# Kernel optimization log

Hardware: AMD Instinct MI355X
Metric: run time of the kernel (lower is better)

The kernel has to match this reference:

```python
import jax, jax.numpy as jnp
import numpy as np

B, T, E, H, V, K = 32, 256, 256, 256, 32000, 48
PAD = 0


def setup_inputs() -> dict:
    key = jax.random.key(0)
    ks = jax.random.split(key, 24)
    lengths = jnp.sort(jax.random.randint(ks[0], (B,), 1, T + 1))[::-1]
    lengths = lengths.at[0].set(T)  # pack_padded needs max length present
    sent = jax.random.randint(ks[1], (B, T), 1, V)
    pos = jnp.arange(T)[None, :]
    sentence = jnp.where(pos < lengths[:, None], sent, PAD)
    tags = jax.random.randint(ks[2], (B, T), 0, K)
    s = 0.1
    p = {"sentence": sentence, "lengths": lengths, "tags": tags}
    p["embed"] = jax.random.normal(ks[3], (V, E)) * s
    dims = [E, 2 * H]
    i = 4
    for l in range(2):
        for d in ("f", "b"):
            p[f"Wih_{l}{d}"] = jax.random.normal(ks[i], (4 * H, dims[l])) * s; i += 1
            p[f"Whh_{l}{d}"] = jax.random.normal(ks[i], (4 * H, H)) * s; i += 1
            p[f"b_{l}{d}"] = jax.random.normal(ks[i], (4 * H,)) * s; i += 1
    p["Wout"] = jax.random.normal(ks[i], (K, 2 * H)) * s; i += 1
    p["bout"] = jax.random.normal(ks[i], (K,)) * s; i += 1
    p["start_t"] = jax.random.normal(ks[i], (K,)) * s; i += 1
    p["end_t"] = jax.random.normal(ks[i], (K,)) * s; i += 1
    p["trans"] = jax.random.normal(ks[i], (K, K)) * s
    return p


def _lstm_dir(x, m, Wih, Whh, b, reverse):
    # x: [T,B,D] time-major, m: [T,B] bool. Masked update emulates pack_padded_sequence.
    if reverse:
        x, m = x[::-1], m[::-1]
    Bn, Hn = x.shape[1], Whh.shape[1]

    def step(carry, inp):
        h, c = carry
        xt, mt = inp
        g = xt @ Wih.T + h @ Whh.T + b
        i_, f_, g_, o_ = jnp.split(g, 4, axis=-1)
        c2 = jax.nn.sigmoid(f_) * c + jax.nn.sigmoid(i_) * jnp.tanh(g_)
        h2 = jax.nn.sigmoid(o_) * jnp.tanh(c2)
        mm = mt[:, None]
        h2 = jnp.where(mm, h2, h)
        c2 = jnp.where(mm, c2, c)
        return (h2, c2), jnp.where(mm, h2, 0.0)

    init = (jnp.zeros((Bn, Hn), x.dtype), jnp.zeros((Bn, Hn), x.dtype))
    _, hs = jax.lax.scan(step, init, (x, m))
    return hs[::-1] if reverse else hs


def _forward(sentence, tags, embed, layer_params, Wout, bout, start_t, end_t, trans):
    mask = sentence != PAD                      # [B,T]
    x = embed[sentence]                          # [B,T,E]
    xt = jnp.transpose(x, (1, 0, 2))             # [T,B,E]
    mt = mask.T                                  # [T,B]
    for (Wf, Uf, bf, Wb, Ub, bb) in layer_params:
        hf = _lstm_dir(xt, mt, Wf, Uf, bf, False)
        hb = _lstm_dir(xt, mt, Wb, Ub, bb, True)
        xt = jnp.concatenate([hf, hb], axis=-1)  # [T,B,2H]
    emit = xt @ Wout.T + bout                    # [T,B,K]; dropout is identity in eval

    # ---- CRF log-likelihood (torchcrf) ----
    mf = mt.astype(emit.dtype)
    tt = tags.T                                  # [T,B]
    bar = jnp.arange(sentence.shape[0])
    num = start_t[tt[0]] + emit[0, bar, tt[0]]

    def num_step(s, inp):
        em, tg, pg, m = inp
        return s + (trans[pg, tg] + em[bar, tg]) * m, None

    num, _ = jax.lax.scan(num_step, num, (emit[1:], tt[1:], tt[:-1], mf[1:]))
    last_idx = mf.sum(0).astype(jnp.int32) - 1
    last_tags = tt[last_idx, bar]
    num = num + end_t[last_tags]

    score = start_t[None, :] + emit[0]           # [B,K]

    def den_step(s, inp):
        em, m = inp
        nxt = jax.nn.logsumexp(s[:, :, None] + trans[None] + em[:, None, :], axis=1)
        return jnp.where(m[:, None] > 0, nxt, s), None

    score, _ = jax.lax.scan(den_step, score, (emit[1:], mf[1:]))
    den = jax.nn.logsumexp(score + end_t[None, :], axis=1)
    loss = (num - den).mean()                    # torchcrf reduction='mean' log-likelihood
    return jnp.transpose(emit, (1, 0, 2)), loss, mask


def reference(sentence, lengths, tags, embed,
              Wih_0f, Whh_0f, b_0f, Wih_0b, Whh_0b, b_0b,
              Wih_1f, Whh_1f, b_1f, Wih_1b, Whh_1b, b_1b,
              Wout, bout, start_t, end_t, trans):
    layers = [(Wih_0f, Whh_0f, b_0f, Wih_0b, Whh_0b, b_0b),
              (Wih_1f, Whh_1f, b_1f, Wih_1b, Whh_1b, b_1b)]
    return _forward(sentence, tags, embed, layers, Wout, bout, start_t, end_t, trans)
```

## Files before the change

kernel.cpp:

```cpp
#include <hip/hip_runtime.h>

#define Bz 32
#define Tz 256
#define Ez 256
#define Hz 256
#define Kz 48
#define G4 1024
#define H2 512

typedef __attribute__((ext_vector_type(8))) short short8;
typedef __attribute__((ext_vector_type(4))) float f32x4;
typedef unsigned short ushort_t;
typedef unsigned int uint_t;
typedef unsigned long long ull_t;

__device__ __forceinline__ float bf2f(ushort_t u) {
    unsigned int x = ((unsigned int)u) << 16;
    union { unsigned int i; float f; } c; c.i = x; return c.f;
}
__device__ __forceinline__ ushort_t f2bf(float f) {
    union { float f; unsigned int i; } c; c.f = f;
    unsigned int x = c.i;
    unsigned int lsb = (x >> 16) & 1u;
    x += 0x7fffu + lsb;
    return (ushort_t)(x >> 16);
}
__device__ __forceinline__ float sigm(float x) { return 1.f / (1.f + __expf(-x)); }
__device__ __forceinline__ float tanh_f(float x) { return 1.f - 2.f / (__expf(2.f * x) + 1.f); }

#define MFMA16(a, b, c) __builtin_amdgcn_mfma_f32_16x16x32_bf16((a), (b), (c), 0, 0, 0)

struct CvtArgs {
    const float* s[9];
    ushort_t* d[9];
    int n[9];
};
__global__ __launch_bounds__(256) void cvt_all(CvtArgs a)
{
    int y = blockIdx.y;
    const float* src = a.s[y];
    ushort_t* dst = a.d[y];
    int n = a.n[y];
    int i = (blockIdx.x * 256 + threadIdx.x) * 4;
    if (i < n) {
        float4 v = *(const float4*)(src + i);
        ushort_t o[4] = { f2bf(v.x), f2bf(v.y), f2bf(v.z), f2bf(v.w) };
        *(uint2*)(dst + i) = *(uint2*)o;
    }
}

__global__ __launch_bounds__(64) void embed_kernel(
    const int* __restrict__ sent, const float* __restrict__ embed,
    ushort_t* __restrict__ emb, float* __restrict__ mask_out)
{
    int blk = blockIdx.x;
    int b = blk >> 8, t = blk & 255;
    int s = sent[blk];
    int tid = threadIdx.x;
    float4 v = *(const float4*)(embed + (size_t)s * Ez + tid * 4);
    ushort_t o[4] = { f2bf(v.x), f2bf(v.y), f2bf(v.z), f2bf(v.w) };
    *(uint2*)(emb + ((size_t)t * Bz + b) * Ez + tid * 4) = *(uint2*)o;
    if (tid == 0) mask_out[blk] = (s != 0) ? 1.0f : 0.0f;
}

__global__ __launch_bounds__(256) void gemm_xproj(
    const ushort_t* __restrict__ A,
    const ushort_t* __restrict__ Wf, const ushort_t* __restrict__ Wb,
    const float* __restrict__ biasf, const float* __restrict__ biasb,
    ushort_t* __restrict__ Cf, ushort_t* __restrict__ Cb,
    int M, int Kd)
{
    const ushort_t* W = blockIdx.z ? Wb : Wf;
    const float* bias = blockIdx.z ? biasb : biasf;
    ushort_t* C = blockIdx.z ? Cb : Cf;
    __shared__ __attribute__((aligned(16))) ushort_t sA[128 * 32];
    __shared__ __attribute__((aligned(16))) ushort_t sB[128 * 32];

    int m0 = blockIdx.x * 128, n0 = blockIdx.y * 128;
    int tid = threadIdx.x, l = tid & 63, w = tid >> 6;
    int lr = l & 15, lq = l >> 4;
    int mw = (w & 1) * 64, nw = (w >> 1) * 64;

    int srow_lane = l >> 2;
    int scol_lane = (l & 3) * 8;

    f32x4 acc[4][4] = {};
    for (int ko = 0; ko < Kd; ko += 32) {
        #pragma unroll
        for (int j = 0; j < 4; j++) {
            int seg = w * 4 + j;
            const ushort_t* src;
            ushort_t* dst;
            if (seg < 8) {
                src = A + (size_t)(m0 + seg * 16 + srow_lane) * Kd + ko + scol_lane;
                dst = sA + seg * 512;
            } else {
                src = W + (size_t)(n0 + (seg - 8) * 16 + srow_lane) * Kd + ko + scol_lane;
                dst = sB + (seg - 8) * 512;
            }
            __builtin_amdgcn_global_load_lds(src, dst, 16, 0, 0);
        }
        asm volatile("s_waitcnt vmcnt(0)" ::: "memory");
        __syncthreads();

        short8 af[4], bf_[4];
        #pragma unroll
        for (int mt = 0; mt < 4; mt++)
            af[mt] = *(const short8*)(&sA[(mw + mt * 16 + lr) * 32 + lq * 8]);
        #pragma unroll
        for (int nt = 0; nt < 4; nt++)
            bf_[nt] = *(const short8*)(&sB[(nw + nt * 16 + lr) * 32 + lq * 8]);
        #pragma unroll
        for (int mt = 0; mt < 4; mt++)
            #pragma unroll
            for (int nt = 0; nt < 4; nt++)
                acc[mt][nt] = MFMA16(af[mt], bf_[nt], acc[mt][nt]);
        __syncthreads();
    }

    #pragma unroll
    for (int mt = 0; mt < 4; mt++)
        #pragma unroll
        for (int nt = 0; nt < 4; nt++)
            #pragma unroll
            for (int r = 0; r < 4; r++) {
                int row = m0 + mw + mt * 16 + lq * 4 + r;
                int col = n0 + nw + nt * 16 + lr;
                float v = acc[mt][nt][r] + bias[col];
                C[(size_t)row * G4 + col] = f2bf(v);
            }
}

#define LDK 264

__global__ __launch_bounds__(256, 1) void lstm_layer(
    const ushort_t* __restrict__ Whh_f, const ushort_t* __restrict__ Whh_b,
    const ushort_t* __restrict__ Xp_f, const ushort_t* __restrict__ Xp_b,
    const int* __restrict__ lengths,
    ushort_t* __restrict__ hcat,
    ull_t* __restrict__ hbuf)
{
    __shared__ __attribute__((aligned(16))) ushort_t sH[Bz][LDK];
    __shared__ float sG[4][16][34];

    int bid = blockIdx.x;
    int dir = bid >> 4;
    int sub = bid & 15;
    int h0 = sub * 16;
    const ushort_t* Whh = dir ? Whh_b : Whh_f;
    const ushort_t* Xp  = dir ? Xp_b  : Xp_f;
    int tid = threadIdx.x, l = tid & 63, w = tid >> 6;
    int lr = l & 15, lq = l >> 4;
    int mw = (w & 1) * 16;
    int P  = w >> 1;
    int U0w = h0 + P * 8;

    short8 bw0[8], bw1[8];
    int gA = (lr & 3) * Hz + U0w + (lr >> 2);
    int gB = gA + 4;
    {
        const ushort_t* W0 = Whh + (size_t)gA * Hz;
        const ushort_t* W1 = Whh + (size_t)gB * Hz;
        #pragma unroll
        for (int k = 0; k < 8; k++) {
            bw0[k] = *(const short8*)(W0 + k * 32 + lq * 8);
            bw1[k] = *(const short8*)(W1 + k * 32 + lq * 8);
        }
    }

    int upd = (l < 32);
    int bloc = l & 15;
    int q = (l >> 4) & 1;
    int batch = mw + bloc;
    int lenb = lengths[batch];
    float c4[4] = {0.f, 0.f, 0.f, 0.f};
    ull_t prevw = 0;
    int pubw = batch * 64 + sub * 4 + P * 2 + q;
    int hcoff = dir * Hz + U0w + q * 4;

    for (int s = 0; s < Tz; s++) {
        int t_act = dir ? (Tz - 1 - s) : s;
        const ushort_t* Xrow = Xp + (size_t)t_act * Bz * G4;

        float xv0[4], xv1[4];
        #pragma unroll
        for (int r = 0; r < 4; r++) {
            int brow = mw + lq * 4 + r;
            xv0[r] = bf2f(Xrow[(size_t)brow * G4 + gA]);
            xv1[r] = bf2f(Xrow[(size_t)brow * G4 + gB]);
        }

        const ull_t* hcur = hbuf + ((s & 1) * 2 + dir) * (Bz * Hz / 4);
        uint_t tagc = (uint_t)(((s >> 1) ^ s) & 1);
        ull_t vals[8];
        uint_t pend = 0xffu;
        while (pend) {
            #pragma unroll
            for (int k = 0; k < 8; k++)
                if (pend & (1u << k))
                    vals[k] = __hip_atomic_load(&hcur[k * 256 + tid],
                                                __ATOMIC_RELAXED, __HIP_MEMORY_SCOPE_AGENT);
            #pragma unroll
            for (int k = 0; k < 8; k++)
                if ((pend & (1u << k)) && (((uint_t)(vals[k] >> 14) & 1u) == tagc))
                    pend &= ~(1u << k);
        }
        #pragma unroll
        for (int k = 0; k < 8; k++) {
            int idx = k * 256 + tid;
            *(ull_t*)(&sH[idx >> 6][(idx & 63) * 4]) = vals[k] & ~(1ull << 14);
        }
        __syncthreads();

        f32x4 acc0 = {}, acc1 = {};
        #pragma unroll
        for (int k = 0; k < 8; k++) {
            short8 a = *(const short8*)(&sH[mw + lr][k * 32 + lq * 8]);
            acc0 = MFMA16(a, bw0[k], acc0);
            acc1 = MFMA16(a, bw1[k], acc1);
        }
        #pragma unroll
        for (int r = 0; r < 4; r++) {
            sG[w][lq * 4 + r][lr]      = acc0[r] + xv0[r];
            sG[w][lq * 4 + r][16 + lr] = acc1[r] + xv1[r];
        }
        asm volatile("s_waitcnt lgkmcnt(0)" ::: "memory");

        uint_t tagp = (uint_t)((((s + 1) >> 1) ^ (s + 1)) & 1);
        if (upd) {
            int msk = (t_act < lenb);
            ushort_t hx[4], hc[4];
            const ushort_t* ho = (const ushort_t*)&prevw;
            #pragma unroll
            for (int j = 0; j < 4; j++) {
                int cb = q * 16 + j * 4;
                float gi = sG[w][bloc][cb], gf = sG[w][bloc][cb + 1];
                float gg = sG[w][bloc][cb + 2], go = sG[w][bloc][cb + 3];
                float c2 = sigm(gf) * c4[j] + sigm(gi) * tanh_f(gg);
                float h2 = sigm(go) * tanh_f(c2);
                if (msk) c4[j] = c2;
                ushort_t hn = f2bf(h2);
                hx[j] = msk ? hn : ho[j];
                hc[j] = msk ? hn : (ushort_t)0;
            }
            ull_t wd; __builtin_memcpy(&wd, hx, 8);
            prevw = wd;
            wd |= ((ull_t)tagp) << 14;
            ull_t* hnxt = hbuf + (((s + 1) & 1) * 2 + dir) * (Bz * Hz / 4);
            __hip_atomic_store(&hnxt[pubw], wd,
                               __ATOMIC_RELAXED, __HIP_MEMORY_SCOPE_AGENT);
            ull_t wc; __builtin_memcpy(&wc, hc, 8);
            *(ull_t*)(hcat + ((size_t)t_act * Bz + batch) * H2 + hcoff) = wc;
        }
    }
}

__global__ __launch_bounds__(256) void gemm_emit(
    const ushort_t* __restrict__ A, const ushort_t* __restrict__ Wout,
    const float* __restrict__ bout, float* __restrict__ emit_out)
{
    int tid = threadIdx.x, l = tid & 63, w = tid >> 6;
    int m0 = blockIdx.x * 64 + w * 16;
    int lr = l & 15, lq = l >> 4;
    f32x4 acc[3] = {};
    for (int ko = 0; ko < H2; ko += 32) {
        short8 a = *(const short8*)(A + (size_t)(m0 + lr) * H2 + ko + lq * 8);
        #pragma unroll
        for (int nt = 0; nt < 3; nt++) {
            short8 bfr = *(const short8*)(Wout + (size_t)(nt * 16 + lr) * H2 + ko + lq * 8);
            acc[nt] = MFMA16(a, bfr, acc[nt]);
        }
    }
    #pragma unroll
    for (int nt = 0; nt < 3; nt++)
        #pragma unroll
        for (int r = 0; r < 4; r++) {
            int row = m0 + lq * 4 + r;
            int col = nt * 16 + lr;
            float v = acc[nt][r] + bout[col];
            int t = row >> 5, b = row & 31;
            emit_out[((size_t)b * Tz + t) * Kz + col] = v;
        }
}

__global__ __launch_bounds__(256) void crf_num(
    const float* __restrict__ emit, const int* __restrict__ sent,
    const int* __restrict__ tags, const int* __restrict__ lengths,
    const float* __restrict__ trans, const float* __restrict__ start_t,
    const float* __restrict__ end_t, float* __restrict__ num)
{
    __shared__ float red[4];
    int b = blockIdx.x, t = threadIdx.x;
    int tg = tags[b * Tz + t];
    float term;
    if (t == 0) {
        term = start_t[tg] + emit[(size_t)b * Tz * Kz + tg];
        int len = lengths[b];
        term += end_t[tags[b * Tz + len - 1]];
    } else if (sent[b * Tz + t] != 0) {
        int tp = tags[b * Tz + t - 1];
        term = trans[tp * Kz + tg] + emit[((size_t)b * Tz + t) * Kz + tg];
    } else term = 0.f;
    #pragma unroll
    for (int off = 1; off < 64; off <<= 1) term += __shfl_xor(term, off);
    int w = t >> 6;
    if ((t & 63) == 0) red[w] = term;
    __syncthreads();
    if (t == 0) num[b] = red[0] + red[1] + red[2] + red[3];
}

__global__ __launch_bounds__(64) void crf_den(
    const float* __restrict__ emit, const int* __restrict__ lengths,
    const float* __restrict__ trans, const float* __restrict__ start_t,
    const float* __restrict__ end_t, float* __restrict__ den)
{
    __shared__ float sT[Kz * Kz];
    __shared__ float sS[Kz];
    int b = blockIdx.x, l = threadIdx.x;
    for (int i = l; i < Kz * Kz; i += 64) sT[i] = trans[i];
    int len = lengths[b];
    bool act = l < Kz;
    float s = act ? (start_t[l] + emit[(size_t)b * Tz * Kz + l]) : -1e30f;
    for (int t = 1; t < len; t++) {
        float em = act ? emit[((size_t)b * Tz + t) * Kz + l] : 0.f;
        if (act) sS[l] = s;
        float M = s;
        #pragma unroll
        for (int off = 1; off < 64; off <<= 1) M = fmaxf(M, __shfl_xor(M, off));
        float a0 = 0.f, a1 = 0.f, a2 = 0.f, a3 = 0.f;
        #pragma unroll 4
        for (int i = 0; i < Kz; i += 4) {
            a0 += __expf(sS[i]     + sT[i * Kz + l]       - M);
            a1 += __expf(sS[i + 1] + sT[(i + 1) * Kz + l] - M);
            a2 += __expf(sS[i + 2] + sT[(i + 2) * Kz + l] - M);
            a3 += __expf(sS[i + 3] + sT[(i + 3) * Kz + l] - M);
        }
        float sum = (a0 + a1) + (a2 + a3);
        if (act) s = em + M + __logf(sum);
    }
    float v = act ? (s + end_t[l]) : -1e30f;
    float M = v;
    #pragma unroll
    for (int off = 1; off < 64; off <<= 1) M = fmaxf(M, __shfl_xor(M, off));
    float accv = act ? __expf(v - M) : 0.f;
    #pragma unroll
    for (int off = 1; off < 64; off <<= 1) accv += __shfl_xor(accv, off);
    if (l == 0) den[b] = M + __logf(accv);
}

__global__ __launch_bounds__(64) void crf_loss(
    const float* __restrict__ num, const float* __restrict__ den, float* __restrict__ out)
{
    int l = threadIdx.x;
    float v = (l < Bz) ? (num[l] - den[l]) : 0.f;
    #pragma unroll
    for (int off = 1; off < 64; off <<= 1) v += __shfl_xor(v, off);
    if (l == 0) out[0] = v / (float)Bz;
}

extern "C" void kernel_launch(void* const* d_in, const int* in_sizes, int n_in,
                              void* d_out, int out_size, void* d_ws, size_t ws_size,
                              hipStream_t stream) {
    const int* sent      = (const int*)d_in[0];
    const int* lengths   = (const int*)d_in[1];
    const int* tags      = (const int*)d_in[2];
    const float* embed   = (const float*)d_in[3];
    const float* Wih0f = (const float*)d_in[4];
    const float* Whh0f = (const float*)d_in[5];
    const float* b0f   = (const float*)d_in[6];
    const float* Wih0b = (const float*)d_in[7];
    const float* Whh0b = (const float*)d_in[8];
    const float* b0b   = (const float*)d_in[9];
    const float* Wih1f = (const float*)d_in[10];
    const float* Whh1f = (const float*)d_in[11];
    const float* b1f   = (const float*)d_in[12];
    const float* Wih1b = (const float*)d_in[13];
    const float* Whh1b = (const float*)d_in[14];
    const float* b1b   = (const float*)d_in[15];
    const float* Wout  = (const float*)d_in[16];
    const float* bout  = (const float*)d_in[17];
    const float* start_t = (const float*)d_in[18];
    const float* end_t   = (const float*)d_in[19];
    const float* trans   = (const float*)d_in[20];

    char* ws = (char*)d_ws;
    ushort_t* Xp_f  = (ushort_t*)(ws);
    ushort_t* Xp_b  = (ushort_t*)(ws + 16777216);
    ushort_t* hcat  = (ushort_t*)(ws + 33554432);
    ushort_t* emb   = (ushort_t*)(ws + 41943040);
    ushort_t* Whh0f_c = (ushort_t*)(ws + 46137344);
    ushort_t* Whh0b_c = (ushort_t*)(ws + 46661632);
    ushort_t* Wih0f_c = (ushort_t*)(ws + 47185920);
    ushort_t* Wih0b_c = (ushort_t*)(ws + 47710208);
    ushort_t* Wih1f_c = (ushort_t*)(ws + 48234496);
    ushort_t* Wih1b_c = (ushort_t*)(ws + 49283072);
    ushort_t* Whh1f_c = (ushort_t*)(ws + 50331648);
    ushort_t* Whh1b_c = (ushort_t*)(ws + 50855936);
    ushort_t* Wout_c  = (ushort_t*)(ws + 51380224);
    ull_t*    hbufL0 = (ull_t*)(ws + 51429376);
    ull_t*    hbufL1 = (ull_t*)(ws + 51560448);
    float*    num   = (float*)   (ws + 51691520);
    float*    den   = (float*)   (ws + 51691776);

    float* out      = (float*)d_out;
    float* loss_out = out + (size_t)Bz * Tz * Kz;
    float* mask_out = loss_out + 1;

    hipMemsetAsync(hbufL0, 0, 262144, stream);

    CvtArgs ca;
    ca.s[0] = Whh0f; ca.d[0] = Whh0f_c; ca.n[0] = 262144;
    ca.s[1] = Whh0b; ca.d[1] = Whh0b_c; ca.n[1] = 262144;
    ca.s[2] = Wih0f; ca.d[2] = Wih0f_c; ca.n[2] = 262144;
    ca.s[3] = Wih0b; ca.d[3] = Wih0b_c; ca.n[3] = 262144;
    ca.s[4] = Wih1f; ca.d[4] = Wih1f_c; ca.n[4] = 524288;
    ca.s[5] = Wih1b; ca.d[5] = Wih1b_c; ca.n[5] = 524288;
    ca.s[6] = Whh1f; ca.d[6] = Whh1f_c; ca.n[6] = 262144;
    ca.s[7] = Whh1b; ca.d[7] = Whh1b_c; ca.n[7] = 262144;
    ca.s[8] = Wout;  ca.d[8] = Wout_c;  ca.n[8] = 24576;
    cvt_all<<<dim3(512, 9), 256, 0, stream>>>(ca);

    embed_kernel<<<Bz * Tz, 64, 0, stream>>>(sent, embed, emb, mask_out);

    gemm_xproj<<<dim3(Tz * Bz / 128, G4 / 128, 2), 256, 0, stream>>>(
        emb, Wih0f_c, Wih0b_c, b0f, b0b, Xp_f, Xp_b, Tz * Bz, Ez);

    lstm_layer<<<32, 256, 0, stream>>>(Whh0f_c, Whh0b_c, Xp_f, Xp_b, lengths, hcat, hbufL0);

    gemm_xproj<<<dim3(Tz * Bz / 128, G4 / 128, 2), 256, 0, stream>>>(
        hcat, Wih1f_c, Wih1b_c, b1f, b1b, Xp_f, Xp_b, Tz * Bz, H2);

    lstm_layer<<<32, 256, 0, stream>>>(Whh1f_c, Whh1b_c, Xp_f, Xp_b, lengths, hcat, hbufL1);

    gemm_emit<<<Tz * Bz / 64, 256, 0, stream>>>(hcat, Wout_c, bout, out);

    crf_num<<<Bz, 256, 0, stream>>>(out, sent, tags, lengths, trans, start_t, end_t, num);
    crf_den<<<Bz, 64, 0, stream>>>(out, lengths, trans, start_t, end_t, den);
    crf_loss<<<1, 64, 0, stream>>>(num, den, loss_out);
}
```

Baseline: 1.877 ms.

## Replace per-word tag polling with per-wave step flags in LSTM recurrence

Cross-block synchronisation of the hidden state switches from spinning on tag bits embedded in every published h word to spinning on two per-wave step-counter flags, then loading h once. Each wave waits for its stores to drain (vmcnt(0)) and lane 0 publishes the step number as a flag. This cuts the polling traffic per thread from eight words to two flags, at the cost of an extra store-drain and flag write per step. Ordering between the h stores and the flag uses relaxed atomics plus a waitcnt rather than a release/acquire pair, so visibility depends on hardware ordering.

```diff
diff --git a/kernel.cpp b/kernel.cpp
--- a/kernel.cpp
+++ b/kernel.cpp
@@ -138,7 +138,8 @@
     const ushort_t* __restrict__ Xp_f, const ushort_t* __restrict__ Xp_b,
     const int* __restrict__ lengths,
     ushort_t* __restrict__ hcat,
-    ull_t* __restrict__ hbuf)
+    ull_t* __restrict__ hbuf,
+    ull_t* __restrict__ flags)
 {
     __shared__ __attribute__((aligned(16))) ushort_t sH[Bz][LDK];
     __shared__ float sG[4][16][34];
@@ -177,6 +178,10 @@
     ull_t prevw = 0;
     int pubw = batch * 64 + sub * 4 + P * 2 + q;
     int hcoff = dir * Hz + U0w + q * 4;
+    int wr = tid & 63;
+    int slotA = (wr & ~3) | (wr & 2);
+    int slotB = slotA + 1;
+    int myflag = sub * 4 + w;
 
     for (int s = 0; s < Tz; s++) {
         int t_act = dir ? (Tz - 1 - s) : s;
@@ -190,25 +195,30 @@
             xv1[r] = bf2f(Xrow[(size_t)brow * G4 + gB]);
         }
 
+        const ull_t* fb = flags + ((s & 1) * 2 + dir) * 64;
+        ull_t se = (ull_t)s;
+        uint_t need = 3u;
+        while (need) {
+            if (need & 1u) {
+                ull_t fA = __hip_atomic_load(&fb[slotA],
+                                             __ATOMIC_RELAXED, __HIP_MEMORY_SCOPE_AGENT);
+                if (fA == se) need &= ~1u;
+            }
+            if (need & 2u) {
+                ull_t fB = __hip_atomic_load(&fb[slotB],
+                                             __ATOMIC_RELAXED, __HIP_MEMORY_SCOPE_AGENT);
+                if (fB == se) need &= ~2u;
+            }
+        }
+        asm volatile("" ::: "memory");
+
         const ull_t* hcur = hbuf + ((s & 1) * 2 + dir) * (Bz * Hz / 4);
-        uint_t tagc = (uint_t)(((s >> 1) ^ s) & 1);
-        ull_t vals[8];
-        uint_t pend = 0xffu;
-        while (pend) {
-            #pragma unroll
-            for (int k = 0; k < 8; k++)
-                if (pend & (1u << k))
-                    vals[k] = __hip_atomic_load(&hcur[k * 256 + tid],
-                                                __ATOMIC_RELAXED, __HIP_MEMORY_SCOPE_AGENT);
-            #pragma unroll
-            for (int k = 0; k < 8; k++)
-                if ((pend & (1u << k)) && (((uint_t)(vals[k] >> 14) & 1u) == tagc))
-                    pend &= ~(1u << k);
-        }
         #pragma unroll
         for (int k = 0; k < 8; k++) {
+            ull_t v = __hip_atomic_load(&hcur[k * 256 + tid],
+                                        __ATOMIC_RELAXED, __HIP_MEMORY_SCOPE_AGENT);
             int idx = k * 256 + tid;
-            *(ull_t*)(&sH[idx >> 6][(idx & 63) * 4]) = vals[k] & ~(1ull << 14);
+            *(ull_t*)(&sH[idx >> 6][(idx & 63) * 4]) = v;
         }
         __syncthreads();
 
@@ -226,7 +236,6 @@
         }
         asm volatile("s_waitcnt lgkmcnt(0)" ::: "memory");
 
-        uint_t tagp = (uint_t)((((s + 1) >> 1) ^ (s + 1)) & 1);
         if (upd) {
             int msk = (t_act < lenb);
             ushort_t hx[4], hc[4];
@@ -245,12 +254,17 @@
             }
             ull_t wd; __builtin_memcpy(&wd, hx, 8);
             prevw = wd;
-            wd |= ((ull_t)tagp) << 14;
             ull_t* hnxt = hbuf + (((s + 1) & 1) * 2 + dir) * (Bz * Hz / 4);
             __hip_atomic_store(&hnxt[pubw], wd,
                                __ATOMIC_RELAXED, __HIP_MEMORY_SCOPE_AGENT);
             ull_t wc; __builtin_memcpy(&wc, hc, 8);
             *(ull_t*)(hcat + ((size_t)t_act * Bz + batch) * H2 + hcoff) = wc;
+        }
+        asm volatile("s_waitcnt vmcnt(0)" ::: "memory");
+        if (l == 0) {
+            ull_t* fn = flags + (((s + 1) & 1) * 2 + dir) * 64;
+            __hip_atomic_store(&fn[myflag], (ull_t)(s + 1),
+                               __ATOMIC_RELAXED, __HIP_MEMORY_SCOPE_AGENT);
         }
     }
 }
@@ -399,14 +413,16 @@
     ushort_t* Wout_c  = (ushort_t*)(ws + 51380224);
     ull_t*    hbufL0 = (ull_t*)(ws + 51429376);
     ull_t*    hbufL1 = (ull_t*)(ws + 51560448);
-    float*    num   = (float*)   (ws + 51691520);
-    float*    den   = (float*)   (ws + 51691776);
+    ull_t*    flagsL0 = (ull_t*)(ws + 51691520);
+    ull_t*    flagsL1 = (ull_t*)(ws + 51693568);
+    float*    num   = (float*)   (ws + 51695616);
+    float*    den   = (float*)   (ws + 51695872);
 
     float* out      = (float*)d_out;
     float* loss_out = out + (size_t)Bz * Tz * Kz;
     float* mask_out = loss_out + 1;
 
-    hipMemsetAsync(hbufL0, 0, 262144, stream);
+    hipMemsetAsync(hbufL0, 0, 266240, stream);
 
     CvtArgs ca;
     ca.s[0] = Whh0f; ca.d[0] = Whh0f_c; ca.n[0] = 262144;
@@ -425,12 +441,12 @@
     gemm_xproj<<<dim3(Tz * Bz / 128, G4 / 128, 2), 256, 0, stream>>>(
         emb, Wih0f_c, Wih0b_c, b0f, b0b, Xp_f, Xp_b, Tz * Bz, Ez);
 
-    lstm_layer<<<32, 256, 0, stream>>>(Whh0f_c, Whh0b_c, Xp_f, Xp_b, lengths, hcat, hbufL0);
+    lstm_layer<<<32, 256, 0, stream>>>(Whh0f_c, Whh0b_c, Xp_f, Xp_b, lengths, hcat, hbufL0, flagsL0);
 
     gemm_xproj<<<dim3(Tz * Bz / 128, G4 / 128, 2), 256, 0, stream>>>(
         hcat, Wih1f_c, Wih1b_c, b1f, b1b, Xp_f, Xp_b, Tz * Bz, H2);
 
-    lstm_layer<<<32, 256, 0, stream>>>(Whh1f_c, Whh1b_c, Xp_f, Xp_b, lengths, hcat, hbufL1);
+    lstm_layer<<<32, 256, 0, stream>>>(Whh1f_c, Whh1b_c, Xp_f, Xp_b, lengths, hcat, hbufL1, flagsL1);
 
     gemm_emit<<<Tz * Bz / 64, 256, 0, stream>>>(hcat, Wout_c, bout, out);
 
```

Result: slower. 3.090 ms (+64.6%).

## Publish hidden state in MFMA fragment layout and poll directly into registers

Applied to the files above, without the earlier changes.

The hidden-state exchange buffer is rearranged so each producer writes its 4-element word at a position matching the MFMA A-operand fragment layout. Each consumer lane now polls its own fragment with wide dwordx4 cache-bypassing loads and feeds them straight to MFMA. This removes the LDS staging array and the per-step __syncthreads. The cost is that each wave spins independently and reloads all eight fragments on every retry, and the tag bit must be checked in two words per fragment.

```diff
diff --git a/kernel.cpp b/kernel.cpp
--- a/kernel.cpp
+++ b/kernel.cpp
@@ -13,6 +13,7 @@
 typedef unsigned short ushort_t;
 typedef unsigned int uint_t;
 typedef unsigned long long ull_t;
+typedef __attribute__((ext_vector_type(4))) uint_t uint4_t;
 
 __device__ __forceinline__ float bf2f(ushort_t u) {
     unsigned int x = ((unsigned int)u) << 16;
@@ -29,6 +30,24 @@
 __device__ __forceinline__ float tanh_f(float x) { return 1.f - 2.f / (__expf(2.f * x) + 1.f); }
 
 #define MFMA16(a, b, c) __builtin_amdgcn_mfma_f32_16x16x32_bf16((a), (b), (c), 0, 0, 0)
+
+__device__ __forceinline__ void pollfrag8(const ull_t* p0, const ull_t* p1, uint4_t* o)
+{
+    asm volatile(
+        "global_load_dwordx4 %0, %8, off sc0 sc1\n\t"
+        "global_load_dwordx4 %1, %8, off offset:1024 sc0 sc1\n\t"
+        "global_load_dwordx4 %2, %8, off offset:2048 sc0 sc1\n\t"
+        "global_load_dwordx4 %3, %8, off offset:3072 sc0 sc1\n\t"
+        "global_load_dwordx4 %4, %9, off sc0 sc1\n\t"
+        "global_load_dwordx4 %5, %9, off offset:1024 sc0 sc1\n\t"
+        "global_load_dwordx4 %6, %9, off offset:2048 sc0 sc1\n\t"
+        "global_load_dwordx4 %7, %9, off offset:3072 sc0 sc1\n\t"
+        "s_waitcnt vmcnt(0)"
+        : "=&v"(o[0]), "=&v"(o[1]), "=&v"(o[2]), "=&v"(o[3]),
+          "=&v"(o[4]), "=&v"(o[5]), "=&v"(o[6]), "=&v"(o[7])
+        : "v"(p0), "v"(p1)
+        : "memory");
+}
 
 struct CvtArgs {
     const float* s[9];
@@ -131,7 +150,7 @@
             }
 }
 
-#define LDK 264
+#define HWRD 2048
 
 __global__ __launch_bounds__(256, 1) void lstm_layer(
     const ushort_t* __restrict__ Whh_f, const ushort_t* __restrict__ Whh_b,
@@ -140,7 +159,6 @@
     ushort_t* __restrict__ hcat,
     ull_t* __restrict__ hbuf)
 {
-    __shared__ __attribute__((aligned(16))) ushort_t sH[Bz][LDK];
     __shared__ float sG[4][16][34];
 
     int bid = blockIdx.x;
@@ -175,8 +193,11 @@
     int lenb = lengths[batch];
     float c4[4] = {0.f, 0.f, 0.f, 0.f};
     ull_t prevw = 0;
-    int pubw = batch * 64 + sub * 4 + P * 2 + q;
+    int g = sub * 4 + P * 2 + q;
+    int pubw = (batch >> 4) * 1024 + (g >> 3) * 128
+             + (batch & 15) * 2 + ((g >> 1) & 3) * 32 + (g & 1);
     int hcoff = dir * Hz + U0w + q * 4;
+    int fbase = (w & 1) * 1024 + l * 2;
 
     for (int s = 0; s < Tz; s++) {
         int t_act = dir ? (Tz - 1 - s) : s;
@@ -190,32 +211,28 @@
             xv1[r] = bf2f(Xrow[(size_t)brow * G4 + gB]);
         }
 
-        const ull_t* hcur = hbuf + ((s & 1) * 2 + dir) * (Bz * Hz / 4);
+        const ull_t* hcur = hbuf + ((s & 1) * 2 + dir) * HWRD;
+        const ull_t* p0 = hcur + fbase;
+        const ull_t* p1 = p0 + 512;
         uint_t tagc = (uint_t)(((s >> 1) ^ s) & 1);
-        ull_t vals[8];
-        uint_t pend = 0xffu;
-        while (pend) {
+        uint4_t fr[8];
+        for (;;) {
+            pollfrag8(p0, p1, fr);
+            uint_t ok = 1u;
             #pragma unroll
             for (int k = 0; k < 8; k++)
-                if (pend & (1u << k))
-                    vals[k] = __hip_atomic_load(&hcur[k * 256 + tid],
-                                                __ATOMIC_RELAXED, __HIP_MEMORY_SCOPE_AGENT);
-            #pragma unroll
-            for (int k = 0; k < 8; k++)
-                if ((pend & (1u << k)) && (((uint_t)(vals[k] >> 14) & 1u) == tagc))
-                    pend &= ~(1u << k);
-        }
+                ok &= (((fr[k].x >> 14) & 1u) == tagc) &
+                      (((fr[k].z >> 14) & 1u) == tagc);
+            if (ok) break;
+        }
+        #pragma unroll
+        for (int k = 0; k < 8; k++) { fr[k].x &= ~0x4000u; fr[k].z &= ~0x4000u; }
+
+        f32x4 acc0 = {}, acc1 = {};
         #pragma unroll
         for (int k = 0; k < 8; k++) {
-            int idx = k * 256 + tid;
-            *(ull_t*)(&sH[idx >> 6][(idx & 63) * 4]) = vals[k] & ~(1ull << 14);
-        }
-        __syncthreads();
-
-        f32x4 acc0 = {}, acc1 = {};
-        #pragma unroll
-        for (int k = 0; k < 8; k++) {
-            short8 a = *(const short8*)(&sH[mw + lr][k * 32 + lq * 8]);
+            short8 a;
+            __builtin_memcpy(&a, &fr[k], 16);
             acc0 = MFMA16(a, bw0[k], acc0);
             acc1 = MFMA16(a, bw1[k], acc1);
         }
@@ -246,7 +263,7 @@
             ull_t wd; __builtin_memcpy(&wd, hx, 8);
             prevw = wd;
             wd |= ((ull_t)tagp) << 14;
-            ull_t* hnxt = hbuf + (((s + 1) & 1) * 2 + dir) * (Bz * Hz / 4);
+            ull_t* hnxt = hbuf + (((s + 1) & 1) * 2 + dir) * HWRD;
             __hip_atomic_store(&hnxt[pubw], wd,
                                __ATOMIC_RELAXED, __HIP_MEMORY_SCOPE_AGENT);
             ull_t wc; __builtin_memcpy(&wc, hc, 8);
```

After: 1.745 ms. 7.0% less time.
